# Optimization experiments

Measured on AMD Instinct MI355X. Metric: run time of the kernel, lower is better.

Reference implementation:

```python
import jax, jax.numpy as jnp
import numpy as np

N = 50000
E = 800000
IN_C = 128
HID = 64
HEADS = 4
NUM_CLASSES = 10
NUM_GRAPHS = 64
EPS = 1e-5
NEG_SLOPE = 0.2


def setup_inputs() -> dict:
    key = jax.random.key(0)
    ks = jax.random.split(key, 32)
    inp = {}
    inp["x"] = jax.random.normal(ks[0], (N, IN_C), dtype=jnp.float32)
    inp["edge_index"] = jax.random.randint(ks[1], (2, E), 0, N, dtype=jnp.int32)
    inp["batch"] = jnp.sort(jax.random.randint(ks[2], (N,), 0, NUM_GRAPHS, dtype=jnp.int32))
    s = 0.05
    # GATConv1: in=128 -> heads=4, hid=64, concat -> 256
    inp["W1"] = jax.random.normal(ks[3], (IN_C, HEADS * HID), dtype=jnp.float32) * s
    inp["a_src1"] = jax.random.normal(ks[4], (HEADS, HID), dtype=jnp.float32) * s
    inp["a_dst1"] = jax.random.normal(ks[5], (HEADS, HID), dtype=jnp.float32) * s
    inp["b1"] = jnp.zeros((HEADS * HID,), dtype=jnp.float32)
    inp["g1"] = jnp.ones((HEADS * HID,), dtype=jnp.float32)
    inp["be1"] = jnp.zeros((HEADS * HID,), dtype=jnp.float32)
    # GATConv2: in=256 -> heads=4, hid=64, concat -> 256
    inp["W2"] = jax.random.normal(ks[6], (HEADS * HID, HEADS * HID), dtype=jnp.float32) * s
    inp["a_src2"] = jax.random.normal(ks[7], (HEADS, HID), dtype=jnp.float32) * s
    inp["a_dst2"] = jax.random.normal(ks[8], (HEADS, HID), dtype=jnp.float32) * s
    inp["b2"] = jnp.zeros((HEADS * HID,), dtype=jnp.float32)
    inp["g2"] = jnp.ones((HEADS * HID,), dtype=jnp.float32)
    inp["be2"] = jnp.zeros((HEADS * HID,), dtype=jnp.float32)
    # GATConv3: in=256 -> heads=1, hid=64, mean (concat=False) -> 64
    inp["W3"] = jax.random.normal(ks[9], (HEADS * HID, 1 * HID), dtype=jnp.float32) * s
    inp["a_src3"] = jax.random.normal(ks[10], (1, HID), dtype=jnp.float32) * s
    inp["a_dst3"] = jax.random.normal(ks[11], (1, HID), dtype=jnp.float32) * s
    inp["b3"] = jnp.zeros((HID,), dtype=jnp.float32)
    inp["g3"] = jnp.ones((HID,), dtype=jnp.float32)
    inp["be3"] = jnp.zeros((HID,), dtype=jnp.float32)
    # final classifier
    inp["fcW"] = jax.random.normal(ks[12], (HID, NUM_CLASSES), dtype=jnp.float32) * s
    inp["fcb"] = jnp.zeros((NUM_CLASSES,), dtype=jnp.float32)
    return inp


def gat_conv(x, src, dst, W, a_src, a_dst, b, heads, out_c, concat):
    # Linear transform, split heads: [N, H, C]
    h = (x @ W).reshape(-1, heads, out_c)
    # Per-node attention logits (dot with per-head attention vectors): [N, H]
    as_ = jnp.einsum("nhc,hc->nh", h, a_src)
    ad_ = jnp.einsum("nhc,hc->nh", h, a_dst)
    # Per-edge unnormalized attention (src contributes a_src, dst a_dst)
    e = jax.nn.leaky_relu(as_[src] + ad_[dst], NEG_SLOPE)  # [E, H]
    # Segment softmax over destination node (stable)
    e_max = jax.ops.segment_max(e, dst, num_segments=N)  # [N, H]
    ex = jnp.exp(e - e_max[dst])
    denom = jax.ops.segment_sum(ex, dst, num_segments=N)  # [N, H]
    alpha = ex / denom[dst]  # [E, H]
    # Weighted scatter-aggregate of source features
    msg = h[src] * alpha[:, :, None]  # [E, H, C]
    out = jax.ops.segment_sum(msg, dst, num_segments=N)  # [N, H, C]
    out = out.reshape(-1, heads * out_c) if concat else out.mean(axis=1)
    return out + b


def batch_norm(x, gamma, beta):
    mean = x.mean(axis=0)
    var = x.var(axis=0)
    return (x - mean) * jax.lax.rsqrt(var + EPS) * gamma + beta


def reference(x, edge_index, batch, W1, a_src1, a_dst1, b1, g1, be1,
              W2, a_src2, a_dst2, b2, g2, be2,
              W3, a_src3, a_dst3, b3, g3, be3, fcW, fcb):
    src, dst = edge_index[0], edge_index[1]
    h = jax.nn.relu(gat_conv(x, src, dst, W1, a_src1, a_dst1, b1, HEADS, HID, True))
    h = batch_norm(h, g1, be1)  # dropout = identity (eval)
    h = jax.nn.relu(gat_conv(h, src, dst, W2, a_src2, a_dst2, b2, HEADS, HID, True))
    h = batch_norm(h, g2, be2)
    h = jax.nn.relu(gat_conv(h, src, dst, W3, a_src3, a_dst3, b3, 1, HID, False))
    h = batch_norm(h, g3, be3)
    # global mean pool over graphs
    sums = jax.ops.segment_sum(h, batch, num_segments=NUM_GRAPHS)  # [G, HID]
    counts = jax.ops.segment_sum(jnp.ones((h.shape[0],), h.dtype), batch, num_segments=NUM_GRAPHS)
    pooled = sums / jnp.maximum(counts, 1.0)[:, None]
    return pooled @ fcW + fcb
```

## Files before the change

### kernel.cpp

```cpp
#include <hip/hip_runtime.h>
#include <hip/hip_bf16.h>

#define N_NODES 50000
#define NUM_E   800000
#define EPS_BN  1e-5f
#define NUM_GRAPHS 64

typedef __attribute__((ext_vector_type(8))) short bf16x8;
typedef __attribute__((ext_vector_type(4))) float f32x4;
typedef unsigned short ushort_t;
typedef unsigned int uint_t;

static __device__ __forceinline__ unsigned short f2bf(float f) {
    unsigned int u = __float_as_uint(f);
    u += 0x7fffu + ((u >> 16) & 1u);
    return (unsigned short)(u >> 16);
}
static __device__ __forceinline__ uint_t pkbf(float lo, float hi) {
    __hip_bfloat162 t = __float22bfloat162_rn(make_float2(lo, hi));
    return *(uint_t*)&t;
}
static __device__ __forceinline__ float bflo(uint_t u) { return __uint_as_float(u << 16); }
static __device__ __forceinline__ float bfhi(uint_t u) { return __uint_as_float(u & 0xffff0000u); }

__global__ void hist_kernel(const int* __restrict__ ei, int* __restrict__ deg) {
    int e = blockIdx.x * blockDim.x + threadIdx.x;
    if (e >= NUM_E) return;
    atomicAdd(&deg[ei[NUM_E + e]], 1);
}

__global__ void scan_local_kernel(const int* __restrict__ deg, int* __restrict__ rowptr,
                                  int* __restrict__ bsum) {
    __shared__ int ws[4];
    int b = blockIdx.x, t = threadIdx.x;
    int i = b * 256 + t;
    int lane = t & 63, wv = t >> 6;
    int v = (i < N_NODES) ? deg[i] : 0;
    int incl = v;
#pragma unroll
    for (int off = 1; off < 64; off <<= 1) {
        int u = __shfl_up(incl, off, 64);
        if (lane >= off) incl += u;
    }
    if (lane == 63) ws[wv] = incl;
    __syncthreads();
    if (t == 0) {
        int s = 0;
#pragma unroll
        for (int k = 0; k < 4; ++k) { int x = ws[k]; ws[k] = s; s += x; }
        bsum[b] = s;
    }
    __syncthreads();
    if (i < N_NODES) rowptr[i + 1] = ws[wv] + incl;
}

__global__ void scan_sums_kernel(int* __restrict__ bsum, int nb) {
    __shared__ int ws[4];
    int t = threadIdx.x;
    int lane = t & 63, wv = t >> 6;
    int v = (t < nb) ? bsum[t] : 0;
    int incl = v;
#pragma unroll
    for (int off = 1; off < 64; off <<= 1) {
        int u = __shfl_up(incl, off, 64);
        if (lane >= off) incl += u;
    }
    if (lane == 63) ws[wv] = incl;
    __syncthreads();
    if (t == 0) {
        int s = 0;
#pragma unroll
        for (int k = 0; k < 4; ++k) { int x = ws[k]; ws[k] = s; s += x; }
    }
    __syncthreads();
    if (t < nb) bsum[t] = ws[wv] + incl - v;
}

__global__ void scan_add_kernel(int* __restrict__ rowptr, const int* __restrict__ bsum) {
    int b = blockIdx.x, t = threadIdx.x;
    int i = b * 256 + t;
    if (i < N_NODES) rowptr[i + 1] += bsum[b];
    if (b == 0 && t == 0) rowptr[0] = 0;
}

__global__ void scatter_kernel(const int* __restrict__ ei, const int* __restrict__ rowptr,
                               int* __restrict__ fill, int* __restrict__ srcs) {
    int e = blockIdx.x * blockDim.x + threadIdx.x;
    if (e >= NUM_E) return;
    int dst = ei[NUM_E + e];
    int pos = rowptr[dst] + atomicAdd(&fill[dst], 1);
    srcs[pos] = ei[e];
}

__global__ void batch_offsets_kernel(const int* __restrict__ batch, int* __restrict__ goff) {
    int g = threadIdx.x;
    if (g > NUM_GRAPHS) return;
    int lo = 0, hi = N_NODES;
    while (lo < hi) {
        int mid = (lo + hi) >> 1;
        if (batch[mid] < g) lo = mid + 1; else hi = mid;
    }
    goff[g] = lo;
}

__global__ void prep_all_kernel(const float* __restrict__ W1, const float* __restrict__ W2,
                                const float* __restrict__ W3, const float* __restrict__ x,
                                ushort_t* __restrict__ w1t, ushort_t* __restrict__ w2t,
                                ushort_t* __restrict__ w3t, ushort_t* __restrict__ xbf) {
    const int S1 = 128 * 256, S2 = 256 * 256, S3 = 256 * 64;
    const int SW = S1 + S2 + S3;
    const int SX = N_NODES * 128 / 4;
    int i = blockIdx.x * blockDim.x + threadIdx.x;
    if (i < SX) {
        float4 v = ((const float4*)x)[i];
        ((uint2*)xbf)[i] = make_uint2(pkbf(v.x, v.y), pkbf(v.z, v.w));
    } else if (i < SX + SW) {
        int j = i - SX;
        if (j < S1) {
            int k = j / 256, n = j % 256;
            w1t[n * 128 + k] = f2bf(W1[j]);
        } else if (j < S1 + S2) {
            int jj = j - S1; int k = jj / 256, n = jj % 256;
            w2t[n * 256 + k] = f2bf(W2[jj]);
        } else {
            int jj = j - S1 - S2; int k = jj / 64, n = jj % 64;
            w3t[n * 256 + k] = f2bf(W3[jj]);
        }
    }
}

template<int K, int NFULL, int BN>
__global__ __launch_bounds__(256) void gemm_fused_kernel(const ushort_t* __restrict__ A,
                                                         const ushort_t* __restrict__ Bt,
                                                         ushort_t* __restrict__ C,
                                                         const float* __restrict__ stats,
                                                         const float* __restrict__ g,
                                                         const float* __restrict__ be,
                                                         const float* __restrict__ a_src,
                                                         const float* __restrict__ a_dst,
                                                         float* __restrict__ as_,
                                                         float* __restrict__ ad_) {
    const int NT = BN / 16;
    const int NG = BN / 64;
    constexpr int LOOP_BYTES = (128 * 40 + BN * 40) * 2;
    constexpr int EPI_BYTES  = 4 * 32 * 64 * 2;
    constexpr int SMEM_BYTES = LOOP_BYTES > EPI_BYTES ? LOOP_BYTES : EPI_BYTES;
    __shared__ __align__(16) unsigned char smem[SMEM_BYTES];
    ushort_t (*As)[40]     = (ushort_t (*)[40])smem;
    ushort_t (*Bs)[40]     = (ushort_t (*)[40])(smem + 128 * 40 * 2);
    ushort_t (*Cs)[32][64] = (ushort_t (*)[32][64])smem;
    __shared__ __align__(16) float aff_a[K], aff_b[K];
    __shared__ float asrc_s[BN], adst_s[BN];
    int tid = threadIdx.x;
    int lane = tid & 63, w = tid >> 6;
    int row0 = blockIdx.x * 128, col0 = blockIdx.y * BN;
    int m_l = lane & 15, q = lane >> 4;

    for (int c = tid; c < K; c += 256) {
        float a = 1.f, b = 0.f;
        if (stats) {
            float m = stats[c] * (1.f / N_NODES);
            float var = fmaxf(stats[256 + c] * (1.f / N_NODES) - m * m, 0.f);
            float rs = rsqrtf(var + EPS_BN) * g[c];
            a = rs; b = be[c] - m * rs;
        }
        aff_a[c] = a; aff_b[c] = b;
    }
    if (tid < BN) {
        asrc_s[tid] = a_src[col0 + tid];
        adst_s[tid] = a_dst[col0 + tid];
    }
    __syncthreads();

    f32x4 acc[2][NT];
#pragma unroll
    for (int r = 0; r < 2; ++r)
#pragma unroll
        for (int c = 0; c < NT; ++c) acc[r][c] = (f32x4){0.f, 0.f, 0.f, 0.f};

    int ar = tid >> 1, ako = (tid & 1) * 16;

    for (int k0 = 0; k0 < K; k0 += 32) {
        uint_t ow[8];
        int gr = row0 + ar;
        uint4 u0 = make_uint4(0, 0, 0, 0), u1 = make_uint4(0, 0, 0, 0);
        if (gr < N_NODES) {
            const ushort_t* ap = A + (long)gr * K + k0 + ako;
            u0 = *(const uint4*)ap;
            u1 = *(const uint4*)(ap + 8);
        }
        uint_t uu[8] = {u0.x, u0.y, u0.z, u0.w, u1.x, u1.y, u1.z, u1.w};
#pragma unroll
        for (int t = 0; t < 8; ++t) {
            int k = k0 + ako + t * 2;
            float lo = bflo(uu[t]) * aff_a[k] + aff_b[k];
            float hi = bfhi(uu[t]) * aff_a[k + 1] + aff_b[k + 1];
            ow[t] = pkbf(lo, hi);
        }
        if constexpr (BN == 128) {
            int br = tid >> 1, bko = (tid & 1) * 16;
            const ushort_t* bp = Bt + (long)(col0 + br) * K + k0 + bko;
            uint4 b0 = *(const uint4*)bp;
            uint4 b1 = *(const uint4*)(bp + 8);
            *(uint4*)&As[ar][ako] = make_uint4(ow[0], ow[1], ow[2], ow[3]);
            *(uint4*)&As[ar][ako + 8] = make_uint4(ow[4], ow[5], ow[6], ow[7]);
            *(uint4*)&Bs[br][bko] = b0;
            *(uint4*)&Bs[br][bko + 8] = b1;
        } else {
            int br = tid >> 2, bko = (tid & 3) * 8;
            uint4 bv = *(const uint4*)(Bt + (long)(col0 + br) * K + k0 + bko);
            *(uint4*)&As[ar][ako] = make_uint4(ow[0], ow[1], ow[2], ow[3]);
            *(uint4*)&As[ar][ako + 8] = make_uint4(ow[4], ow[5], ow[6], ow[7]);
            *(uint4*)&Bs[br][bko] = bv;
        }
        __syncthreads();

        bf16x8 af[2];
#pragma unroll
        for (int r = 0; r < 2; ++r)
            af[r] = *(const bf16x8*)&As[w * 32 + r * 16 + m_l][q * 8];
#pragma unroll
        for (int c = 0; c < NT; ++c) {
            bf16x8 bf = *(const bf16x8*)&Bs[c * 16 + m_l][q * 8];
#pragma unroll
            for (int r = 0; r < 2; ++r)
                acc[r][c] = __builtin_amdgcn_mfma_f32_16x16x32_bf16(af[r], bf, acc[r][c], 0, 0, 0);
        }
        __syncthreads();
    }

    const int H = NFULL / 64;
#pragma unroll
    for (int gblk = 0; gblk < NG; ++gblk) {
        int hidx = blockIdx.y * NG + gblk;
        int colg = col0 + gblk * 64;
#pragma unroll
        for (int r = 0; r < 2; ++r)
#pragma unroll
            for (int cc = 0; cc < 4; ++cc)
#pragma unroll
                for (int i = 0; i < 4; ++i)
                    Cs[w][r * 16 + q * 4 + i][cc * 16 + m_l] = f2bf(acc[r][gblk * 4 + cc][i]);
#pragma unroll
        for (int j = 0; j < 4; ++j) {
            int flat = j * 64 + lane;
            int lr = flat >> 3, chg = flat & 7;
            int gr = row0 + w * 32 + lr;
            uint4 u = *(uint4*)&Cs[w][lr][chg * 8];
            float f0 = bflo(u.x), f1 = bfhi(u.x), f2 = bflo(u.y), f3 = bfhi(u.y);
            float f4 = bflo(u.z), f5 = bfhi(u.z), f6 = bflo(u.w), f7 = bfhi(u.w);
            int cb = gblk * 64 + chg * 8;
            float s1 = f0 * asrc_s[cb] + f1 * asrc_s[cb + 1] + f2 * asrc_s[cb + 2] + f3 * asrc_s[cb + 3]
                     + f4 * asrc_s[cb + 4] + f5 * asrc_s[cb + 5] + f6 * asrc_s[cb + 6] + f7 * asrc_s[cb + 7];
            float s2 = f0 * adst_s[cb] + f1 * adst_s[cb + 1] + f2 * adst_s[cb + 2] + f3 * adst_s[cb + 3]
                     + f4 * adst_s[cb + 4] + f5 * adst_s[cb + 5] + f6 * adst_s[cb + 6] + f7 * adst_s[cb + 7];
#pragma unroll
            for (int o = 1; o < 8; o <<= 1) {
                s1 += __shfl_xor(s1, o, 64);
                s2 += __shfl_xor(s2, o, 64);
            }
            if (gr < N_NODES) {
                *(uint4*)(C + (long)gr * NFULL + colg + chg * 8) = u;
                if ((lane & 7) == 0) {
                    as_[gr * H + hidx] = s1;
                    ad_[gr * H + hidx] = s2;
                }
            }
        }
    }
}

__global__ __launch_bounds__(256) void agg4_kernel(const ushort_t* __restrict__ h,
                                                   const float* __restrict__ as_,
                                                   const float* __restrict__ ad_,
                                                   const int* __restrict__ rowptr,
                                                   const int* __restrict__ srcs,
                                                   const float* __restrict__ bias,
                                                   ushort_t* __restrict__ out) {
    __shared__ float alds[4][256];
    int lane = threadIdx.x & 63, w = threadIdx.x >> 6;
    int q = lane >> 4, cl = lane & 15;
    int n = blockIdx.x * 16 + w * 4 + q;
    if (n >= N_NODES) return;
    int start = rowptr[n];
    int deg = rowptr[n + 1] - start;

    float4 adv = *(const float4*)(ad_ + n * 4);
    float ad4[4] = {adv.x, adv.y, adv.z, adv.w};

    float mx[4] = {-1e30f, -1e30f, -1e30f, -1e30f};
    float dn[4] = {0.f, 0.f, 0.f, 0.f};
    int s0reg = 0;
    {
        float vst[4] = {-1e30f, -1e30f, -1e30f, -1e30f};
        if (deg > 0) s0reg = srcs[start + min(cl, deg - 1)];
        if (cl < deg) {
            float4 av = *(const float4*)(as_ + s0reg * 4);
            float vv[4] = {av.x + ad4[0], av.y + ad4[1], av.z + ad4[2], av.w + ad4[3]};
#pragma unroll
            for (int hh = 0; hh < 4; ++hh) {
                float v = vv[hh] > 0.f ? vv[hh] : 0.2f * vv[hh];
                vst[hh] = v; mx[hh] = v; dn[hh] = 1.f;
            }
        }
        *(float4*)&alds[w][lane * 4] = make_float4(vst[0], vst[1], vst[2], vst[3]);
        for (int j = cl + 16; j < deg; j += 16) {
            int s = srcs[start + j];
            float4 av = *(const float4*)(as_ + s * 4);
            float vv[4] = {av.x + ad4[0], av.y + ad4[1], av.z + ad4[2], av.w + ad4[3]};
#pragma unroll
            for (int hh = 0; hh < 4; ++hh) {
                float v = vv[hh] > 0.f ? vv[hh] : 0.2f * vv[hh];
                float mn = fmaxf(mx[hh], v);
                dn[hh] = dn[hh] * __expf(mx[hh] - mn) + __expf(v - mn);
                mx[hh] = mn;
            }
        }
    }
    float mloc[4] = {mx[0], mx[1], mx[2], mx[3]};
#pragma unroll
    for (int off = 1; off < 16; off <<= 1)
#pragma unroll
        for (int hh = 0; hh < 4; ++hh) mx[hh] = fmaxf(mx[hh], __shfl_xor(mx[hh], off, 64));
#pragma unroll
    for (int hh = 0; hh < 4; ++hh) dn[hh] *= __expf(mloc[hh] - mx[hh]);
#pragma unroll
    for (int off = 1; off < 16; off <<= 1)
#pragma unroll
        for (int hh = 0; hh < 4; ++hh) dn[hh] += __shfl_xor(dn[hh], off, 64);
    float inv[4];
#pragma unroll
    for (int hh = 0; hh < 4; ++hh) inv[hh] = dn[hh] > 0.f ? 1.f / dn[hh] : 0.f;

    {
        float4 vv = *(const float4*)&alds[w][lane * 4];
        float4 al;
        al.x = __expf(vv.x - mx[0]) * inv[0];
        al.y = __expf(vv.y - mx[1]) * inv[1];
        al.z = __expf(vv.z - mx[2]) * inv[2];
        al.w = __expf(vv.w - mx[3]) * inv[3];
        *(float4*)&alds[w][lane * 4] = al;
    }

    int hd = cl >> 2;
    float acc[16];
#pragma unroll
    for (int k = 0; k < 16; ++k) acc[k] = 0.f;
    for (int chunk = 0; chunk < deg || chunk == 0; chunk += 16) {
        int s = s0reg;
        if (chunk > 0) {
            int j = chunk + cl;
            float4 al = make_float4(0.f, 0.f, 0.f, 0.f);
            s = srcs[start + min(j, deg - 1)];
            if (j < deg) {
                float4 av = *(const float4*)(as_ + s * 4);
                float vv[4] = {av.x + ad4[0], av.y + ad4[1], av.z + ad4[2], av.w + ad4[3]};
                float a4[4];
#pragma unroll
                for (int hh = 0; hh < 4; ++hh) {
                    float v = vv[hh] > 0.f ? vv[hh] : 0.2f * vv[hh];
                    a4[hh] = __expf(v - mx[hh]) * inv[hh];
                }
                al = make_float4(a4[0], a4[1], a4[2], a4[3]);
            }
            *(float4*)&alds[w][lane * 4] = al;
        }
        int cnt = min(16, deg - chunk);
        if (cnt < 0) cnt = 0;
#pragma unroll 4
        for (int e = 0; e < cnt; ++e) {
            int se = __shfl(s, q * 16 + e, 64);
            float al = alds[w][(q * 16 + e) * 4 + hd];
            const ushort_t* hr = h + (long)se * 256 + cl * 16;
            uint4 u0 = *(const uint4*)hr;
            uint4 u1 = *(const uint4*)(hr + 8);
            acc[0] += al * bflo(u0.x);  acc[1] += al * bfhi(u0.x);
            acc[2] += al * bflo(u0.y);  acc[3] += al * bfhi(u0.y);
            acc[4] += al * bflo(u0.z);  acc[5] += al * bfhi(u0.z);
            acc[6] += al * bflo(u0.w);  acc[7] += al * bfhi(u0.w);
            acc[8] += al * bflo(u1.x);  acc[9] += al * bfhi(u1.x);
            acc[10] += al * bflo(u1.y); acc[11] += al * bfhi(u1.y);
            acc[12] += al * bflo(u1.z); acc[13] += al * bfhi(u1.z);
            acc[14] += al * bflo(u1.w); acc[15] += al * bfhi(u1.w);
        }
        if (deg <= 16) break;
    }
    int c0 = cl * 16;
    uint_t ow[8];
#pragma unroll
    for (int t = 0; t < 8; ++t) {
        float lo = fmaxf(acc[t * 2] + bias[c0 + t * 2], 0.f);
        float hi = fmaxf(acc[t * 2 + 1] + bias[c0 + t * 2 + 1], 0.f);
        ow[t] = pkbf(lo, hi);
    }
    ushort_t* op = out + (long)n * 256 + c0;
    *(uint4*)op = make_uint4(ow[0], ow[1], ow[2], ow[3]);
    *(uint4*)(op + 8) = make_uint4(ow[4], ow[5], ow[6], ow[7]);
}

__global__ __launch_bounds__(256) void agg1_kernel(const ushort_t* __restrict__ h,
                                                   const float* __restrict__ as_,
                                                   const float* __restrict__ ad_,
                                                   const int* __restrict__ rowptr,
                                                   const int* __restrict__ srcs,
                                                   const float* __restrict__ bias,
                                                   ushort_t* __restrict__ out) {
    __shared__ float alds1[4][64];
    int lane = threadIdx.x & 63, w = threadIdx.x >> 6;
    int o = lane >> 3, cl = lane & 7;
    int n = blockIdx.x * 32 + w * 8 + o;
    if (n >= N_NODES) return;
    int start = rowptr[n];
    int deg = rowptr[n + 1] - start;
    float adn = ad_[n];

    float mx = -1e30f, dn = 0.f;
    int s0reg = 0;
    {
        float vst = -1e30f;
        if (deg > 0) s0reg = srcs[start + min(cl, deg - 1)];
        if (cl < deg) {
            float v = as_[s0reg] + adn;
            v = v > 0.f ? v : 0.2f * v;
            vst = v; mx = v; dn = 1.f;
        }
        alds1[w][lane] = vst;
        for (int j = cl + 8; j < deg; j += 8) {
            int s = srcs[start + j];
            float v = as_[s] + adn;
            v = v > 0.f ? v : 0.2f * v;
            float mn = fmaxf(mx, v);
            dn = dn * __expf(mx - mn) + __expf(v - mn);
            mx = mn;
        }
    }
    float mloc = mx;
#pragma unroll
    for (int off = 1; off < 8; off <<= 1) mx = fmaxf(mx, __shfl_xor(mx, off, 64));
    dn *= __expf(mloc - mx);
#pragma unroll
    for (int off = 1; off < 8; off <<= 1) dn += __shfl_xor(dn, off, 64);
    float inv = dn > 0.f ? 1.f / dn : 0.f;

    alds1[w][lane] = __expf(alds1[w][lane] - mx) * inv;

    float acc[8] = {0.f, 0.f, 0.f, 0.f, 0.f, 0.f, 0.f, 0.f};
    for (int chunk = 0; chunk < deg || chunk == 0; chunk += 8) {
        int s = s0reg;
        if (chunk > 0) {
            int j = chunk + cl;
            float al = 0.f;
            s = srcs[start + min(j, deg - 1)];
            if (j < deg) {
                float v = as_[s] + adn;
                v = v > 0.f ? v : 0.2f * v;
                al = __expf(v - mx) * inv;
            }
            alds1[w][lane] = al;
        }
        int cnt = min(8, deg - chunk);
        if (cnt < 0) cnt = 0;
#pragma unroll 4
        for (int e = 0; e < cnt; ++e) {
            int se = __shfl(s, o * 8 + e, 64);
            float al = alds1[w][o * 8 + e];
            const ushort_t* hr = h + (long)se * 64 + cl * 8;
            uint4 u = *(const uint4*)hr;
            acc[0] += al * bflo(u.x); acc[1] += al * bfhi(u.x);
            acc[2] += al * bflo(u.y); acc[3] += al * bfhi(u.y);
            acc[4] += al * bflo(u.z); acc[5] += al * bfhi(u.z);
            acc[6] += al * bflo(u.w); acc[7] += al * bfhi(u.w);
        }
        if (deg <= 8) break;
    }
    int c0 = cl * 8;
    uint_t ow[4];
#pragma unroll
    for (int t = 0; t < 4; ++t) {
        float lo = fmaxf(acc[t * 2] + bias[c0 + t * 2], 0.f);
        float hi = fmaxf(acc[t * 2 + 1] + bias[c0 + t * 2 + 1], 0.f);
        ow[t] = pkbf(lo, hi);
    }
    *(uint4*)(out + (long)n * 64 + c0) = make_uint4(ow[0], ow[1], ow[2], ow[3]);
}

template<int C>
__global__ __launch_bounds__(256) void bn_stats_bf16(const ushort_t* __restrict__ x,
                                                     float* __restrict__ stats) {
    const int GROUPS = C / 8;
    const int RS = 256 / GROUPS;
    int tid = threadIdx.x;
    int cg_ = tid % GROUPS;
    int rs = tid / GROUPS;
    float s[8], s2[8];
#pragma unroll
    for (int k = 0; k < 8; ++k) { s[k] = 0.f; s2[k] = 0.f; }
    for (int n = blockIdx.x * RS + rs; n < N_NODES; n += gridDim.x * RS) {
        uint4 u = *(const uint4*)(x + (long)n * C + cg_ * 8);
        float f[8] = {bflo(u.x), bfhi(u.x), bflo(u.y), bfhi(u.y),
                      bflo(u.z), bfhi(u.z), bflo(u.w), bfhi(u.w)};
#pragma unroll
        for (int k = 0; k < 8; ++k) { s[k] += f[k]; s2[k] += f[k] * f[k]; }
    }
    __shared__ float red[256][16];
#pragma unroll
    for (int k = 0; k < 8; ++k) { red[tid][k] = s[k]; red[tid][8 + k] = s2[k]; }
    __syncthreads();
    if (tid < C) {
        int g = tid >> 3, k = tid & 7;
        float a = 0.f, b = 0.f;
        for (int r = 0; r < RS; ++r) {
            a += red[g + r * GROUPS][k];
            b += red[g + r * GROUPS][8 + k];
        }
        atomicAdd(&stats[tid], a);
        atomicAdd(&stats[256 + tid], b);
    }
}

__global__ __launch_bounds__(256) void pool_fc_kernel(const ushort_t* __restrict__ h,
                                                      const int* __restrict__ goff,
                                                      const float* __restrict__ stats,
                                                      const float* __restrict__ g3,
                                                      const float* __restrict__ be3,
                                                      const float* __restrict__ fcW,
                                                      const float* __restrict__ fcb,
                                                      float* __restrict__ out) {
    int g = blockIdx.x;
    int c = threadIdx.x & 63;
    int ty = threadIdx.x >> 6;
    int s = goff[g], e = goff[g + 1];
    float sum = 0.f;
    for (int n = s + ty; n < e; n += 4) sum += bflo((uint_t)h[(long)n * 64 + c]);
    __shared__ float red[4][64];
    __shared__ float pv[64];
    red[ty][c] = sum;
    __syncthreads();
    if (ty == 0) {
        float tot = red[0][c] + red[1][c] + red[2][c] + red[3][c];
        float v = tot / fmaxf((float)(e - s), 1.f);
        float m = stats[c] * (1.f / N_NODES);
        float var = fmaxf(stats[256 + c] * (1.f / N_NODES) - m * m, 0.f);
        pv[c] = (v - m) * rsqrtf(var + EPS_BN) * g3[c] + be3[c];
    }
    __syncthreads();
    if (threadIdx.x < 10) {
        int j = threadIdx.x;
        float acc = fcb[j];
#pragma unroll
        for (int k = 0; k < 64; ++k) acc += pv[k] * fcW[k * 10 + j];
        out[g * 10 + j] = acc;
    }
}

extern "C" void kernel_launch(void* const* d_in, const int* in_sizes, int n_in,
                              void* d_out, int out_size, void* d_ws, size_t ws_size,
                              hipStream_t stream) {
    const float* x      = (const float*)d_in[0];
    const int*   ei     = (const int*)d_in[1];
    const int*   batch  = (const int*)d_in[2];
    const float* W1     = (const float*)d_in[3];
    const float* a_src1 = (const float*)d_in[4];
    const float* a_dst1 = (const float*)d_in[5];
    const float* b1     = (const float*)d_in[6];
    const float* g1     = (const float*)d_in[7];
    const float* be1    = (const float*)d_in[8];
    const float* W2     = (const float*)d_in[9];
    const float* a_src2 = (const float*)d_in[10];
    const float* a_dst2 = (const float*)d_in[11];
    const float* b2     = (const float*)d_in[12];
    const float* g2     = (const float*)d_in[13];
    const float* be2    = (const float*)d_in[14];
    const float* W3     = (const float*)d_in[15];
    const float* a_src3 = (const float*)d_in[16];
    const float* a_dst3 = (const float*)d_in[17];
    const float* b3     = (const float*)d_in[18];
    const float* g3     = (const float*)d_in[19];
    const float* be3    = (const float*)d_in[20];
    const float* fcW    = (const float*)d_in[21];
    const float* fcb    = (const float*)d_in[22];
    float* out = (float*)d_out;

    const size_t N = N_NODES, E = NUM_E;
    ushort_t* hbf    = (ushort_t*)d_ws;
    ushort_t* hagg   = hbf + N * 256;
    ushort_t* xbf    = hagg + N * 256;
    ushort_t* w1t    = xbf + N * 128;
    ushort_t* w2t    = w1t + 256 * 128;
    ushort_t* w3t    = w2t + 256 * 256;
    float*    as_    = (float*)(w3t + 64 * 256 + 128);
    float*    ad_    = as_ + N * 4;
    int*      deg    = (int*)(ad_ + N * 4);
    int*      fill   = deg + N;
    float*    statsA = (float*)(fill + N);
    float*    statsB = statsA + 512;
    float*    statsC = statsB + 512;
    int*      rowptr = (int*)(statsC + 512);
    int*      srcs   = rowptr + (N + 1);
    int*      bsum   = srcs + E;
    int*      goff   = bsum + 256;

    const int NB = (N_NODES + 255) / 256;

    hipMemsetAsync(deg, 0, sizeof(int) * (2 * N + 3 * 512), stream);
    hist_kernel<<<(NUM_E + 255) / 256, 256, 0, stream>>>(ei, deg);
    scan_local_kernel<<<NB, 256, 0, stream>>>(deg, rowptr, bsum);
    scan_sums_kernel<<<1, 256, 0, stream>>>(bsum, NB);
    scan_add_kernel<<<NB, 256, 0, stream>>>(rowptr, bsum);
    scatter_kernel<<<(NUM_E + 255) / 256, 256, 0, stream>>>(ei, rowptr, fill, srcs);
    batch_offsets_kernel<<<1, 128, 0, stream>>>(batch, goff);
    prep_all_kernel<<<(N_NODES * 128 / 4 + 128 * 256 + 256 * 256 + 256 * 64 + 255) / 256, 256, 0, stream>>>(
        W1, W2, W3, x, w1t, w2t, w3t, xbf);

    const int GB = (N_NODES + 127) / 128;

    gemm_fused_kernel<128, 256, 128><<<dim3(GB, 2), 256, 0, stream>>>(
        xbf, w1t, hbf, nullptr, nullptr, nullptr, a_src1, a_dst1, as_, ad_);
    agg4_kernel<<<(N_NODES + 15) / 16, 256, 0, stream>>>(hbf, as_, ad_, rowptr, srcs, b1, hagg);
    bn_stats_bf16<256><<<128, 256, 0, stream>>>(hagg, statsA);

    gemm_fused_kernel<256, 256, 128><<<dim3(GB, 2), 256, 0, stream>>>(
        hagg, w2t, hbf, statsA, g1, be1, a_src2, a_dst2, as_, ad_);
    agg4_kernel<<<(N_NODES + 15) / 16, 256, 0, stream>>>(hbf, as_, ad_, rowptr, srcs, b2, hagg);
    bn_stats_bf16<256><<<128, 256, 0, stream>>>(hagg, statsB);

    gemm_fused_kernel<256, 64, 64><<<dim3(GB, 1), 256, 0, stream>>>(
        hagg, w3t, hbf, statsB, g2, be2, a_src3, a_dst3, as_, ad_);
    agg1_kernel<<<(N_NODES + 31) / 32, 256, 0, stream>>>(hbf, as_, ad_, rowptr, srcs, b3, hagg);
    bn_stats_bf16<64><<<128, 256, 0, stream>>>(hagg, statsC);

    pool_fc_kernel<<<NUM_GRAPHS, 256, 0, stream>>>(hagg, goff, statsC, g3, be3, fcW, fcb, out);
}
```

Baseline: 507.0 us.

## Fuse BN statistics into aggregation and split 4-head aggregation across two head-pair blocks

Removes the three separate bn_stats passes by computing per-channel sum and sum-of-squares in the aggregation epilogue: a wave shuffle reduction, then shared-memory atomics, then global atomics. The 4-head aggregation is also split along a second grid dimension so each block handles two heads (128 channels), halving per-thread accumulators and doubling parallelism. The cost is that each split block recomputes edge indices and softmax max/denominator work, and every block issues extra atomics. The 4-head launch uses N/16 blocks without bounds checks, which relies on N being divisible by 16.

```diff
diff --git a/kernel.cpp b/kernel.cpp
--- a/kernel.cpp
+++ b/kernel.cpp
@@ -270,132 +270,139 @@
     }
 }
 
-__global__ __launch_bounds__(256) void agg4_kernel(const ushort_t* __restrict__ h,
-                                                   const float* __restrict__ as_,
-                                                   const float* __restrict__ ad_,
-                                                   const int* __restrict__ rowptr,
-                                                   const int* __restrict__ srcs,
-                                                   const float* __restrict__ bias,
-                                                   ushort_t* __restrict__ out) {
-    __shared__ float alds[4][256];
-    int lane = threadIdx.x & 63, w = threadIdx.x >> 6;
+__global__ __launch_bounds__(256) void agg4h_kernel(const ushort_t* __restrict__ h,
+                                                    const float* __restrict__ as_,
+                                                    const float* __restrict__ ad_,
+                                                    const int* __restrict__ rowptr,
+                                                    const int* __restrict__ srcs,
+                                                    const float* __restrict__ bias,
+                                                    ushort_t* __restrict__ out,
+                                                    float* __restrict__ stats) {
+    __shared__ float alds[4][132];
+    __shared__ float ssum[128], ssq[128];
+    int tid = threadIdx.x;
+    int lane = tid & 63, w = tid >> 6;
     int q = lane >> 4, cl = lane & 15;
+    int y = blockIdx.y;
     int n = blockIdx.x * 16 + w * 4 + q;
-    if (n >= N_NODES) return;
+    for (int i = tid; i < 128; i += 256) { ssum[i] = 0.f; ssq[i] = 0.f; }
+    __syncthreads();
+
     int start = rowptr[n];
     int deg = rowptr[n + 1] - start;
-
-    float4 adv = *(const float4*)(ad_ + n * 4);
-    float ad4[4] = {adv.x, adv.y, adv.z, adv.w};
-
-    float mx[4] = {-1e30f, -1e30f, -1e30f, -1e30f};
-    float dn[4] = {0.f, 0.f, 0.f, 0.f};
+    float2 adv = *(const float2*)(ad_ + n * 4 + 2 * y);
+    float ad0 = adv.x, ad1 = adv.y;
+
+    float mx0 = -1e30f, mx1 = -1e30f, dn0 = 0.f, dn1 = 0.f;
     int s0reg = 0;
     {
-        float vst[4] = {-1e30f, -1e30f, -1e30f, -1e30f};
+        float v0 = -1e30f, v1 = -1e30f;
         if (deg > 0) s0reg = srcs[start + min(cl, deg - 1)];
         if (cl < deg) {
-            float4 av = *(const float4*)(as_ + s0reg * 4);
-            float vv[4] = {av.x + ad4[0], av.y + ad4[1], av.z + ad4[2], av.w + ad4[3]};
-#pragma unroll
-            for (int hh = 0; hh < 4; ++hh) {
-                float v = vv[hh] > 0.f ? vv[hh] : 0.2f * vv[hh];
-                vst[hh] = v; mx[hh] = v; dn[hh] = 1.f;
-            }
-        }
-        *(float4*)&alds[w][lane * 4] = make_float4(vst[0], vst[1], vst[2], vst[3]);
+            float2 av = *(const float2*)(as_ + s0reg * 4 + 2 * y);
+            v0 = av.x + ad0; v0 = v0 > 0.f ? v0 : 0.2f * v0;
+            v1 = av.y + ad1; v1 = v1 > 0.f ? v1 : 0.2f * v1;
+            mx0 = v0; dn0 = 1.f; mx1 = v1; dn1 = 1.f;
+        }
+        *(float2*)&alds[w][q * 33 + cl * 2] = make_float2(v0, v1);
         for (int j = cl + 16; j < deg; j += 16) {
             int s = srcs[start + j];
-            float4 av = *(const float4*)(as_ + s * 4);
-            float vv[4] = {av.x + ad4[0], av.y + ad4[1], av.z + ad4[2], av.w + ad4[3]};
-#pragma unroll
-            for (int hh = 0; hh < 4; ++hh) {
-                float v = vv[hh] > 0.f ? vv[hh] : 0.2f * vv[hh];
-                float mn = fmaxf(mx[hh], v);
-                dn[hh] = dn[hh] * __expf(mx[hh] - mn) + __expf(v - mn);
-                mx[hh] = mn;
-            }
-        }
-    }
-    float mloc[4] = {mx[0], mx[1], mx[2], mx[3]};
-#pragma unroll
-    for (int off = 1; off < 16; off <<= 1)
-#pragma unroll
-        for (int hh = 0; hh < 4; ++hh) mx[hh] = fmaxf(mx[hh], __shfl_xor(mx[hh], off, 64));
-#pragma unroll
-    for (int hh = 0; hh < 4; ++hh) dn[hh] *= __expf(mloc[hh] - mx[hh]);
-#pragma unroll
-    for (int off = 1; off < 16; off <<= 1)
-#pragma unroll
-        for (int hh = 0; hh < 4; ++hh) dn[hh] += __shfl_xor(dn[hh], off, 64);
-    float inv[4];
-#pragma unroll
-    for (int hh = 0; hh < 4; ++hh) inv[hh] = dn[hh] > 0.f ? 1.f / dn[hh] : 0.f;
-
+            float2 av = *(const float2*)(as_ + s * 4 + 2 * y);
+            float u0 = av.x + ad0; u0 = u0 > 0.f ? u0 : 0.2f * u0;
+            float u1 = av.y + ad1; u1 = u1 > 0.f ? u1 : 0.2f * u1;
+            float m0 = fmaxf(mx0, u0);
+            dn0 = dn0 * __expf(mx0 - m0) + __expf(u0 - m0); mx0 = m0;
+            float m1 = fmaxf(mx1, u1);
+            dn1 = dn1 * __expf(mx1 - m1) + __expf(u1 - m1); mx1 = m1;
+        }
+    }
+    float ml0 = mx0, ml1 = mx1;
+#pragma unroll
+    for (int off = 1; off < 16; off <<= 1) {
+        mx0 = fmaxf(mx0, __shfl_xor(mx0, off, 64));
+        mx1 = fmaxf(mx1, __shfl_xor(mx1, off, 64));
+    }
+    dn0 *= __expf(ml0 - mx0); dn1 *= __expf(ml1 - mx1);
+#pragma unroll
+    for (int off = 1; off < 16; off <<= 1) {
+        dn0 += __shfl_xor(dn0, off, 64);
+        dn1 += __shfl_xor(dn1, off, 64);
+    }
+    float inv0 = dn0 > 0.f ? 1.f / dn0 : 0.f;
+    float inv1 = dn1 > 0.f ? 1.f / dn1 : 0.f;
     {
-        float4 vv = *(const float4*)&alds[w][lane * 4];
-        float4 al;
-        al.x = __expf(vv.x - mx[0]) * inv[0];
-        al.y = __expf(vv.y - mx[1]) * inv[1];
-        al.z = __expf(vv.z - mx[2]) * inv[2];
-        al.w = __expf(vv.w - mx[3]) * inv[3];
-        *(float4*)&alds[w][lane * 4] = al;
-    }
-
-    int hd = cl >> 2;
-    float acc[16];
-#pragma unroll
-    for (int k = 0; k < 16; ++k) acc[k] = 0.f;
+        float2 vv = *(float2*)&alds[w][q * 33 + cl * 2];
+        *(float2*)&alds[w][q * 33 + cl * 2] =
+            make_float2(__expf(vv.x - mx0) * inv0, __expf(vv.y - mx1) * inv1);
+    }
+
+    int hd = cl >> 3;
+    int c0 = cl * 8;
+    float acc[8];
+#pragma unroll
+    for (int k = 0; k < 8; ++k) acc[k] = 0.f;
     for (int chunk = 0; chunk < deg || chunk == 0; chunk += 16) {
         int s = s0reg;
         if (chunk > 0) {
             int j = chunk + cl;
-            float4 al = make_float4(0.f, 0.f, 0.f, 0.f);
+            float a0 = 0.f, a1 = 0.f;
             s = srcs[start + min(j, deg - 1)];
             if (j < deg) {
-                float4 av = *(const float4*)(as_ + s * 4);
-                float vv[4] = {av.x + ad4[0], av.y + ad4[1], av.z + ad4[2], av.w + ad4[3]};
-                float a4[4];
-#pragma unroll
-                for (int hh = 0; hh < 4; ++hh) {
-                    float v = vv[hh] > 0.f ? vv[hh] : 0.2f * vv[hh];
-                    a4[hh] = __expf(v - mx[hh]) * inv[hh];
-                }
-                al = make_float4(a4[0], a4[1], a4[2], a4[3]);
+                float2 av = *(const float2*)(as_ + s * 4 + 2 * y);
+                float u0 = av.x + ad0; u0 = u0 > 0.f ? u0 : 0.2f * u0;
+                float u1 = av.y + ad1; u1 = u1 > 0.f ? u1 : 0.2f * u1;
+                a0 = __expf(u0 - mx0) * inv0;
+                a1 = __expf(u1 - mx1) * inv1;
             }
-            *(float4*)&alds[w][lane * 4] = al;
+            *(float2*)&alds[w][q * 33 + cl * 2] = make_float2(a0, a1);
         }
         int cnt = min(16, deg - chunk);
         if (cnt < 0) cnt = 0;
-#pragma unroll 4
+#pragma unroll 8
         for (int e = 0; e < cnt; ++e) {
             int se = __shfl(s, q * 16 + e, 64);
-            float al = alds[w][(q * 16 + e) * 4 + hd];
-            const ushort_t* hr = h + (long)se * 256 + cl * 16;
-            uint4 u0 = *(const uint4*)hr;
-            uint4 u1 = *(const uint4*)(hr + 8);
-            acc[0] += al * bflo(u0.x);  acc[1] += al * bfhi(u0.x);
-            acc[2] += al * bflo(u0.y);  acc[3] += al * bfhi(u0.y);
-            acc[4] += al * bflo(u0.z);  acc[5] += al * bfhi(u0.z);
-            acc[6] += al * bflo(u0.w);  acc[7] += al * bfhi(u0.w);
-            acc[8] += al * bflo(u1.x);  acc[9] += al * bfhi(u1.x);
-            acc[10] += al * bflo(u1.y); acc[11] += al * bfhi(u1.y);
-            acc[12] += al * bflo(u1.z); acc[13] += al * bfhi(u1.z);
-            acc[14] += al * bflo(u1.w); acc[15] += al * bfhi(u1.w);
+            float al = alds[w][q * 33 + e * 2 + hd];
+            const ushort_t* hr = h + (long)se * 256 + y * 128 + c0;
+            uint4 u = *(const uint4*)hr;
+            acc[0] += al * bflo(u.x); acc[1] += al * bfhi(u.x);
+            acc[2] += al * bflo(u.y); acc[3] += al * bfhi(u.y);
+            acc[4] += al * bflo(u.z); acc[5] += al * bfhi(u.z);
+            acc[6] += al * bflo(u.w); acc[7] += al * bfhi(u.w);
         }
         if (deg <= 16) break;
     }
-    int c0 = cl * 16;
-    uint_t ow[8];
-#pragma unroll
-    for (int t = 0; t < 8; ++t) {
-        float lo = fmaxf(acc[t * 2] + bias[c0 + t * 2], 0.f);
-        float hi = fmaxf(acc[t * 2 + 1] + bias[c0 + t * 2 + 1], 0.f);
-        ow[t] = pkbf(lo, hi);
-    }
-    ushort_t* op = out + (long)n * 256 + c0;
-    *(uint4*)op = make_uint4(ow[0], ow[1], ow[2], ow[3]);
-    *(uint4*)(op + 8) = make_uint4(ow[4], ow[5], ow[6], ow[7]);
+
+    int cg = y * 128 + c0;
+    float v[8];
+#pragma unroll
+    for (int t = 0; t < 8; ++t) v[t] = fmaxf(acc[t] + bias[cg + t], 0.f);
+    uint_t ow[4];
+#pragma unroll
+    for (int t = 0; t < 4; ++t) ow[t] = pkbf(v[2 * t], v[2 * t + 1]);
+    *(uint4*)(out + (long)n * 256 + cg) = make_uint4(ow[0], ow[1], ow[2], ow[3]);
+
+    float s1[8], s2[8];
+#pragma unroll
+    for (int t = 0; t < 8; ++t) { s1[t] = v[t]; s2[t] = v[t] * v[t]; }
+#pragma unroll
+    for (int off = 16; off < 64; off <<= 1)
+#pragma unroll
+        for (int t = 0; t < 8; ++t) {
+            s1[t] += __shfl_xor(s1[t], off, 64);
+            s2[t] += __shfl_xor(s2[t], off, 64);
+        }
+    if (lane < 16) {
+#pragma unroll
+        for (int t = 0; t < 8; ++t) {
+            atomicAdd(&ssum[c0 + t], s1[t]);
+            atomicAdd(&ssq[c0 + t], s2[t]);
+        }
+    }
+    __syncthreads();
+    if (tid < 128) {
+        atomicAdd(&stats[y * 128 + tid], ssum[tid]);
+        atomicAdd(&stats[256 + y * 128 + tid], ssq[tid]);
+    }
 }
 
 __global__ __launch_bounds__(256) void agg1_kernel(const ushort_t* __restrict__ h,
@@ -404,15 +411,22 @@
                                                    const int* __restrict__ rowptr,
                                                    const int* __restrict__ srcs,
                                                    const float* __restrict__ bias,
-                                                   ushort_t* __restrict__ out) {
+                                                   ushort_t* __restrict__ out,
+                                                   float* __restrict__ stats) {
     __shared__ float alds1[4][64];
-    int lane = threadIdx.x & 63, w = threadIdx.x >> 6;
+    __shared__ float ssum[64], ssq[64];
+    int tid = threadIdx.x;
+    int lane = tid & 63, w = tid >> 6;
     int o = lane >> 3, cl = lane & 7;
     int n = blockIdx.x * 32 + w * 8 + o;
-    if (n >= N_NODES) return;
-    int start = rowptr[n];
-    int deg = rowptr[n + 1] - start;
-    float adn = ad_[n];
+    bool valid = n < N_NODES;
+    int nc = valid ? n : N_NODES - 1;
+    if (tid < 64) { ssum[tid] = 0.f; ssq[tid] = 0.f; }
+    __syncthreads();
+
+    int start = rowptr[nc];
+    int deg = valid ? rowptr[nc + 1] - start : 0;
+    float adn = ad_[nc];
 
     float mx = -1e30f, dn = 0.f;
     int s0reg = 0;
@@ -474,47 +488,39 @@
         if (deg <= 8) break;
     }
     int c0 = cl * 8;
-    uint_t ow[4];
-#pragma unroll
-    for (int t = 0; t < 4; ++t) {
-        float lo = fmaxf(acc[t * 2] + bias[c0 + t * 2], 0.f);
-        float hi = fmaxf(acc[t * 2 + 1] + bias[c0 + t * 2 + 1], 0.f);
-        ow[t] = pkbf(lo, hi);
-    }
-    *(uint4*)(out + (long)n * 64 + c0) = make_uint4(ow[0], ow[1], ow[2], ow[3]);
-}
-
-template<int C>
-__global__ __launch_bounds__(256) void bn_stats_bf16(const ushort_t* __restrict__ x,
-                                                     float* __restrict__ stats) {
-    const int GROUPS = C / 8;
-    const int RS = 256 / GROUPS;
-    int tid = threadIdx.x;
-    int cg_ = tid % GROUPS;
-    int rs = tid / GROUPS;
-    float s[8], s2[8];
-#pragma unroll
-    for (int k = 0; k < 8; ++k) { s[k] = 0.f; s2[k] = 0.f; }
-    for (int n = blockIdx.x * RS + rs; n < N_NODES; n += gridDim.x * RS) {
-        uint4 u = *(const uint4*)(x + (long)n * C + cg_ * 8);
-        float f[8] = {bflo(u.x), bfhi(u.x), bflo(u.y), bfhi(u.y),
-                      bflo(u.z), bfhi(u.z), bflo(u.w), bfhi(u.w)};
-#pragma unroll
-        for (int k = 0; k < 8; ++k) { s[k] += f[k]; s2[k] += f[k] * f[k]; }
-    }
-    __shared__ float red[256][16];
-#pragma unroll
-    for (int k = 0; k < 8; ++k) { red[tid][k] = s[k]; red[tid][8 + k] = s2[k]; }
-    __syncthreads();
-    if (tid < C) {
-        int g = tid >> 3, k = tid & 7;
-        float a = 0.f, b = 0.f;
-        for (int r = 0; r < RS; ++r) {
-            a += red[g + r * GROUPS][k];
-            b += red[g + r * GROUPS][8 + k];
-        }
-        atomicAdd(&stats[tid], a);
-        atomicAdd(&stats[256 + tid], b);
+    float v[8];
+#pragma unroll
+    for (int t = 0; t < 8; ++t) v[t] = fmaxf(acc[t] + bias[c0 + t], 0.f);
+    if (valid) {
+        uint_t ow[4];
+#pragma unroll
+        for (int t = 0; t < 4; ++t) ow[t] = pkbf(v[2 * t], v[2 * t + 1]);
+        *(uint4*)(out + (long)n * 64 + c0) = make_uint4(ow[0], ow[1], ow[2], ow[3]);
+    }
+    float s1[8], s2[8];
+#pragma unroll
+    for (int t = 0; t < 8; ++t) {
+        s1[t] = valid ? v[t] : 0.f;
+        s2[t] = valid ? v[t] * v[t] : 0.f;
+    }
+#pragma unroll
+    for (int off = 8; off < 64; off <<= 1)
+#pragma unroll
+        for (int t = 0; t < 8; ++t) {
+            s1[t] += __shfl_xor(s1[t], off, 64);
+            s2[t] += __shfl_xor(s2[t], off, 64);
+        }
+    if (lane < 8) {
+#pragma unroll
+        for (int t = 0; t < 8; ++t) {
+            atomicAdd(&ssum[c0 + t], s1[t]);
+            atomicAdd(&ssq[c0 + t], s2[t]);
+        }
+    }
+    __syncthreads();
+    if (tid < 64) {
+        atomicAdd(&stats[tid], ssum[tid]);
+        atomicAdd(&stats[256 + tid], ssq[tid]);
     }
 }
 
@@ -613,21 +619,19 @@
         W1, W2, W3, x, w1t, w2t, w3t, xbf);
 
     const int GB = (N_NODES + 127) / 128;
+    const int AB = N_NODES / 16;
 
     gemm_fused_kernel<128, 256, 128><<<dim3(GB, 2), 256, 0, stream>>>(
         xbf, w1t, hbf, nullptr, nullptr, nullptr, a_src1, a_dst1, as_, ad_);
-    agg4_kernel<<<(N_NODES + 15) / 16, 256, 0, stream>>>(hbf, as_, ad_, rowptr, srcs, b1, hagg);
-    bn_stats_bf16<256><<<128, 256, 0, stream>>>(hagg, statsA);
+    agg4h_kernel<<<dim3(AB, 2), 256, 0, stream>>>(hbf, as_, ad_, rowptr, srcs, b1, hagg, statsA);
 
     gemm_fused_kernel<256, 256, 128><<<dim3(GB, 2), 256, 0, stream>>>(
         hagg, w2t, hbf, statsA, g1, be1, a_src2, a_dst2, as_, ad_);
-    agg4_kernel<<<(N_NODES + 15) / 16, 256, 0, stream>>>(hbf, as_, ad_, rowptr, srcs, b2, hagg);
-    bn_stats_bf16<256><<<128, 256, 0, stream>>>(hagg, statsB);
+    agg4h_kernel<<<dim3(AB, 2), 256, 0, stream>>>(hbf, as_, ad_, rowptr, srcs, b2, hagg, statsB);
 
     gemm_fused_kernel<256, 64, 64><<<dim3(GB, 1), 256, 0, stream>>>(
         hagg, w3t, hbf, statsB, g2, be2, a_src3, a_dst3, as_, ad_);
-    agg1_kernel<<<(N_NODES + 31) / 32, 256, 0, stream>>>(hbf, as_, ad_, rowptr, srcs, b3, hagg);
-    bn_stats_bf16<64><<<128, 256, 0, stream>>>(hagg, statsC);
+    agg1_kernel<<<(N_NODES + 31) / 32, 256, 0, stream>>>(hbf, as_, ad_, rowptr, srcs, b3, hagg, statsC);
 
     pool_fc_kernel<<<NUM_GRAPHS, 256, 0, stream>>>(hagg, goff, statsC, g3, be3, fcW, fcb, out);
 }
```

Result: slower. 683.1 us (+34.7%).
